# Kernel tuning notes

Measured on AMD Instinct MI355X. Metric: run time of the kernel, lower is better.

Reference implementation:

```python
import jax, jax.numpy as jnp
import numpy as np

LOC = 200 * 200 + 1   # location vocab
E = 100               # loc_emb_size
H = 100               # hidden_neurons (== input size of STLSTM)
D = 12                # temporal/spatial slot embedding dim
NSLOT = 92


def setup_inputs() -> dict:
    key = jax.random.key(0)
    ks = jax.random.split(key, 24)
    B, T = 1024, 256
    inp = {}
    inp["traj"] = jax.random.randint(ks[0], (B, T), 0, LOC)
    inp["lennew"] = jax.random.randint(ks[1], (B, T), 0, T)
    inp["traj_len"] = 255  # static scalar (loop runs traj_len+1 steps)
    inp["tu"] = jax.random.randint(ks[2], (B, T), 0, NSLOT)
    inp["tl"] = jax.random.randint(ks[3], (B, T), 0, NSLOT)
    inp["tu_slot"] = jax.random.randint(ks[4], (B, T), 0, NSLOT)
    inp["tl_slot"] = jax.random.randint(ks[5], (B, T), 0, NSLOT)
    inp["su"] = jax.random.randint(ks[6], (B, T), 0, NSLOT)
    inp["sl"] = jax.random.randint(ks[7], (B, T), 0, NSLOT)
    inp["su_slot"] = jax.random.randint(ks[8], (B, T), 0, NSLOT)
    inp["sl_slot"] = jax.random.randint(ks[9], (B, T), 0, NSLOT)
    # learned parameters
    inp["emb_loc"] = jax.random.normal(ks[10], (LOC, E), jnp.float32) * 0.02
    inp["emb_t"] = jax.random.normal(ks[11], (NSLOT, D), jnp.float32) * 0.02
    inp["emb_s"] = jax.random.normal(ks[12], (NSLOT, D), jnp.float32) * 0.02
    inp["W_ih"] = jax.random.normal(ks[13], (E, 4 * H), jnp.float32) * 0.05
    inp["W_hh"] = jax.random.normal(ks[14], (H, 4 * H), jnp.float32) * 0.05
    inp["b"] = jnp.zeros((4 * H,), jnp.float32)
    inp["W_xt"] = jax.random.normal(ks[15], (E, H), jnp.float32) * 0.05
    inp["W_tt"] = jax.random.normal(ks[16], (D, H), jnp.float32) * 0.05
    inp["b_t"] = jnp.zeros((H,), jnp.float32)
    inp["W_xs"] = jax.random.normal(ks[17], (E, H), jnp.float32) * 0.05
    inp["W_ss"] = jax.random.normal(ks[18], (D, H), jnp.float32) * 0.05
    inp["b_s"] = jnp.zeros((H,), jnp.float32)
    return inp


def reference(traj, lennew, traj_len, tu, tl, tu_slot, tl_slot, su, sl,
              su_slot, sl_slot, emb_loc, emb_t, emb_s, W_ih, W_hh, b,
              W_xt, W_tt, b_t, W_xs, W_ss, b_s):
    steps = int(traj_len) + 1  # static python int -> static slice
    x = emb_loc[traj[:, :steps]]            # [B, S, E] (dropout is identity in eval)
    dtype = x.dtype

    def interp(up_e, low_e, up_d, low_d):
        # linear interpolation between upper/lower slot embeddings
        up = up_d[:, :steps].astype(dtype)[..., None]
        low = low_d[:, :steps].astype(dtype)[..., None]
        return (up * low_e + low * up_e) / jnp.maximum(up + low, 1.0)

    Tq = interp(emb_t[tu[:, :steps]], emb_t[tl[:, :steps]], tu_slot, tl_slot)  # [B,S,D]
    Sq = interp(emb_s[su[:, :steps]], emb_s[sl[:, :steps]], su_slot, sl_slot)  # [B,S,D]

    B = traj.shape[0]
    h0 = jnp.zeros((B, H), dtype)
    c0 = jnp.zeros((B, H), dtype)
    xs = (x.swapaxes(0, 1), Tq.swapaxes(0, 1), Sq.swapaxes(0, 1))  # time-major

    def step(carry, inp):
        h, c = carry
        xt, tg, sg = inp
        gates = xt @ W_ih + h @ W_hh + b           # [B, 4H]
        i, f, g, o = jnp.split(gates, 4, axis=-1)
        i = jax.nn.sigmoid(i)
        f = jax.nn.sigmoid(f)
        g = jnp.tanh(g)
        o = jax.nn.sigmoid(o)
        tgate = jax.nn.sigmoid(xt @ W_xt + tg @ W_tt + b_t)  # temporal gate
        sgate = jax.nn.sigmoid(xt @ W_xs + sg @ W_ss + b_s)  # spatial gate
        c = f * c + i * tgate * sgate * g
        h = o * jnp.tanh(c)
        return (h, c), None

    (h, c), _ = jax.lax.scan(step, (h0, c0), xs)
    # model returns h at index traj_len, which is the final hidden state
    return h
```

## Files before the change

kernel.cpp:

```cpp
#include <hip/hip_runtime.h>

#define B_    1024
#define T_    256
#define LOCN  40001
#define E_    100
#define H_    100
#define NC    600

constexpr int PROWS = 16;
constexpr int PPAD  = 20;

__global__ __launch_bounds__(320) void proj_loc_kernel(
    const float* __restrict__ emb_loc,
    const float* __restrict__ W_ih,
    const float* __restrict__ W_xt,
    const float* __restrict__ W_xs,
    const float* __restrict__ b,
    const float* __restrict__ b_t,
    const float* __restrict__ b_s,
    float* __restrict__ P)
{
    __shared__ __attribute__((aligned(16))) float aT[E_][PPAD];
    const int tid  = threadIdx.x;
    const int row0 = blockIdx.x * PROWS;

    for (int i = tid; i < PROWS * E_; i += 320) {
        int r = i / E_, k = i - r * E_;
        int rr = row0 + r;
        float v = 0.f;
        if (rr < LOCN) v = emb_loc[rr * E_ + k];
        aT[k][r] = v;
    }
    __syncthreads();
    if (tid >= 300) return;

    for (int cc = 0; cc < 2; ++cc) {
        const int c = tid + cc * 300;
        const float* wp; int stride; float bias;
        if (c < 400)      { wp = W_ih + c;         stride = 400; bias = b[c]; }
        else if (c < 500) { wp = W_xt + (c - 400); stride = 100; bias = b_t[c - 400]; }
        else              { wp = W_xs + (c - 500); stride = 100; bias = b_s[c - 500]; }

        float acc[PROWS];
        #pragma unroll
        for (int r = 0; r < PROWS; ++r) acc[r] = bias;

        for (int k = 0; k < E_; ++k) {
            float w = wp[(size_t)k * stride];
            #pragma unroll
            for (int r = 0; r < PROWS; ++r) acc[r] += aT[k][r] * w;
        }
        #pragma unroll
        for (int r = 0; r < PROWS; ++r) {
            int rr = row0 + r;
            if (rr < LOCN) P[(size_t)rr * NC + c] = acc[r];
        }
    }
}

__global__ void proj_ts_kernel(
    const float* __restrict__ emb_t, const float* __restrict__ emb_s,
    const float* __restrict__ W_tt,  const float* __restrict__ W_ss,
    float* __restrict__ P_t, float* __restrict__ P_s)
{
    int idx = blockIdx.x * 256 + threadIdx.x;
    if (idx >= 2 * 92 * H_) return;
    int which = idx / (92 * H_);
    int rem   = idx - which * (92 * H_);
    int r = rem / H_, c = rem - r * H_;
    const float* e = which ? emb_s : emb_t;
    const float* W = which ? W_ss : W_tt;
    float acc = 0.f;
    #pragma unroll
    for (int k = 0; k < 12; ++k) acc += e[r * 12 + k] * W[k * H_ + c];
    (which ? P_s : P_t)[rem] = acc;
}

constexpr int RB = 4;
constexpr int NT = 704;

__global__ __launch_bounds__(NT, 3) void lstm_rec_kernel(
    const int* __restrict__ traj,
    const int* __restrict__ traj_len_p,
    const int* __restrict__ tu,      const int* __restrict__ tl,
    const int* __restrict__ tu_slot, const int* __restrict__ tl_slot,
    const int* __restrict__ su,      const int* __restrict__ sl,
    const int* __restrict__ su_slot, const int* __restrict__ sl_slot,
    const float* __restrict__ P,
    const float* __restrict__ P_t,
    const float* __restrict__ P_s,
    const float* __restrict__ W_hh,
    float* __restrict__ out)
{
    __shared__ __attribute__((aligned(16))) float h_lds[RB][H_];
    __shared__ float gates_lds[RB][400];
    __shared__ float tg_lds[RB][H_];
    __shared__ float sg_lds[RB][H_];
    __shared__ int   loc_lds[2][RB];

    const int tid = threadIdx.x;
    const int b0  = blockIdx.x * RB;
    int steps = traj_len_p[0] + 1;
    if (steps > T_) steps = T_;

    float w[H_];
    if (tid < 400) {
        #pragma unroll
        for (int k = 0; k < H_; ++k) w[k] = W_hh[k * 400 + tid];
        ((float*)h_lds)[tid] = 0.f;
    }
    if (tid < RB) loc_lds[0][tid] = traj[(b0 + tid) * T_];

    const int er = tid / 100;
    const int eh = tid - er * 100;
    float c_reg = 0.f, hval = 0.f;
    __syncthreads();

    for (int t = 0; t < steps; ++t) {
        const int buf = t & 1;

        if (tid >= 700) {
            int r = tid - 700;
            if (t + 1 < steps) loc_lds[buf ^ 1][r] = traj[(b0 + r) * T_ + t + 1];
        }

        if (tid < 400) {
            const int n = tid;
            float gacc[RB];
            #pragma unroll
            for (int r = 0; r < RB; ++r)
                gacc[r] = P[(size_t)loc_lds[buf][r] * NC + n];

            float acc[RB] = {0.f, 0.f, 0.f, 0.f};
            #pragma unroll
            for (int k4 = 0; k4 < H_ / 4; ++k4) {
                #pragma unroll
                for (int r = 0; r < RB; ++r) {
                    float4 hv = *(const float4*)(&h_lds[r][k4 * 4]);
                    acc[r] += hv.x * w[k4 * 4 + 0];
                    acc[r] += hv.y * w[k4 * 4 + 1];
                    acc[r] += hv.z * w[k4 * 4 + 2];
                    acc[r] += hv.w * w[k4 * 4 + 3];
                }
            }
            const bool isg = (n >= 200 && n < 300);
            #pragma unroll
            for (int r = 0; r < RB; ++r) {
                float v  = acc[r] + gacc[r];
                float xx = isg ? 2.f * v : v;
                float s  = 1.f / (1.f + expf(-xx));
                gates_lds[r][n] = isg ? (2.f * s - 1.f) : s;
            }
        }

        if (tid >= 448 && tid < 648) {
            const int  ch   = tid - 448;
            const bool is_t = ch < 100;
            const int  hx   = is_t ? ch : ch - 100;
            const int* up_a = is_t ? tu_slot : su_slot;
            const int* lo_a = is_t ? tl_slot : sl_slot;
            const int* ui_a = is_t ? tu : su;
            const int* li_a = is_t ? tl : sl;
            const float* Pq = is_t ? P_t : P_s;
            float* dst      = is_t ? &tg_lds[0][0] : &sg_lds[0][0];
            #pragma unroll
            for (int r = 0; r < RB; ++r) {
                const int off = (b0 + r) * T_ + t;
                float gp  = P[(size_t)loc_lds[buf][r] * NC + 400 + ch];
                float up  = (float)up_a[off];
                float low = (float)lo_a[off];
                int   ui  = ui_a[off], li = li_a[off];
                float iv  = (up * Pq[li * H_ + hx] + low * Pq[ui * H_ + hx])
                            / fmaxf(up + low, 1.f);
                float pre = gp + iv;
                dst[r * H_ + hx] = 1.f / (1.f + expf(-pre));
            }
        }
        __syncthreads();

        if (tid < 400) {
            float i_g = gates_lds[er][eh];
            float f_g = gates_lds[er][100 + eh];
            float g_g = gates_lds[er][200 + eh];
            float o_g = gates_lds[er][300 + eh];
            float tsg = tg_lds[er][eh] * sg_lds[er][eh];
            c_reg = f_g * c_reg + i_g * tsg * g_g;
            hval  = o_g * tanhf(c_reg);
            h_lds[er][eh] = hval;
        }
        __syncthreads();
    }

    if (tid < 400) out[b0 * H_ + tid] = hval;
}

extern "C" void kernel_launch(void* const* d_in, const int* in_sizes, int n_in,
                              void* d_out, int out_size, void* d_ws, size_t ws_size,
                              hipStream_t stream) {
    const int*   traj     = (const int*)  d_in[0];
    const int*   traj_len = (const int*)  d_in[2];
    const int*   tu       = (const int*)  d_in[3];
    const int*   tl       = (const int*)  d_in[4];
    const int*   tu_slot  = (const int*)  d_in[5];
    const int*   tl_slot  = (const int*)  d_in[6];
    const int*   su       = (const int*)  d_in[7];
    const int*   sl       = (const int*)  d_in[8];
    const int*   su_slot  = (const int*)  d_in[9];
    const int*   sl_slot  = (const int*)  d_in[10];
    const float* emb_loc  = (const float*)d_in[11];
    const float* emb_t    = (const float*)d_in[12];
    const float* emb_s    = (const float*)d_in[13];
    const float* W_ih     = (const float*)d_in[14];
    const float* W_hh     = (const float*)d_in[15];
    const float* b        = (const float*)d_in[16];
    const float* W_xt     = (const float*)d_in[17];
    const float* W_tt     = (const float*)d_in[18];
    const float* b_t      = (const float*)d_in[19];
    const float* W_xs     = (const float*)d_in[20];
    const float* W_ss     = (const float*)d_in[21];
    const float* b_s      = (const float*)d_in[22];

    float* P   = (float*)d_ws;
    float* P_t = P + (size_t)LOCN * NC;
    float* P_s = P_t + 92 * H_;

    proj_loc_kernel<<<(LOCN + PROWS - 1) / PROWS, 320, 0, stream>>>(
        emb_loc, W_ih, W_xt, W_xs, b, b_t, b_s, P);
    proj_ts_kernel<<<(2 * 92 * H_ + 255) / 256, 256, 0, stream>>>(
        emb_t, emb_s, W_tt, W_ss, P_t, P_s);
    lstm_rec_kernel<<<B_ / RB, NT, 0, stream>>>(
        traj, traj_len, tu, tl, tu_slot, tl_slot, su, sl, su_slot, sl_slot,
        P, P_t, P_s, W_hh, (float*)d_out);
}
```

Before: 830.2 us.

## Compute recurrent W_hh matvec with split-bf16 MFMA and interleave gate columns

```diff
diff --git a/kernel.cpp b/kernel.cpp
--- a/kernel.cpp
+++ b/kernel.cpp
@@ -7,16 +7,29 @@
 #define H_    100
 #define NC    600
 
+typedef __attribute__((ext_vector_type(8))) short short8;
+typedef __attribute__((ext_vector_type(4))) float f32x4;
+
+__device__ __forceinline__ float fsig(float x)  { return 1.f / (1.f + __expf(-x)); }
+__device__ __forceinline__ float ftanh(float x) { return 2.f / (1.f + __expf(-2.f * x)) - 1.f; }
+
+__device__ __forceinline__ unsigned short bf16_rne(float f) {
+    unsigned int u = __float_as_uint(f);
+    unsigned int r = u + 0x7fffu + ((u >> 16) & 1u);
+    return (unsigned short)(r >> 16);
+}
+__device__ __forceinline__ float bf16_to_f(unsigned short h) {
+    return __uint_as_float(((unsigned int)h) << 16);
+}
+
 constexpr int PROWS = 16;
 constexpr int PPAD  = 20;
 
 __global__ __launch_bounds__(320) void proj_loc_kernel(
     const float* __restrict__ emb_loc,
-    const float* __restrict__ W_ih,
-    const float* __restrict__ W_xt,
+    const float* __restrict__ W_ih, const float* __restrict__ W_xt,
     const float* __restrict__ W_xs,
-    const float* __restrict__ b,
-    const float* __restrict__ b_t,
+    const float* __restrict__ b, const float* __restrict__ b_t,
     const float* __restrict__ b_s,
     float* __restrict__ P)
 {
@@ -50,10 +63,11 @@
             #pragma unroll
             for (int r = 0; r < PROWS; ++r) acc[r] += aT[k][r] * w;
         }
+        const int cs = (c < 400) ? ((c % 100) * 4 + c / 100) : c;
         #pragma unroll
         for (int r = 0; r < PROWS; ++r) {
             int rr = row0 + r;
-            if (rr < LOCN) P[(size_t)rr * NC + c] = acc[r];
+            if (rr < LOCN) P[(size_t)rr * NC + cs] = acc[r];
         }
     }
 }
@@ -77,9 +91,10 @@
 }
 
 constexpr int RB = 4;
-constexpr int NT = 704;
-
-__global__ __launch_bounds__(NT, 3) void lstm_rec_kernel(
+constexpr int NT = 1024;
+
+__global__ __launch_bounds__(NT, 4)
+void lstm_rec_kernel(
     const int* __restrict__ traj,
     const int* __restrict__ traj_len_p,
     const int* __restrict__ tu,      const int* __restrict__ tl,
@@ -92,23 +107,44 @@
     const float* __restrict__ W_hh,
     float* __restrict__ out)
 {
-    __shared__ __attribute__((aligned(16))) float h_lds[RB][H_];
+    __shared__ __attribute__((aligned(16))) unsigned int afH32[4 * 64 * 4];
+    __shared__ __attribute__((aligned(16))) unsigned int afL32[4 * 64 * 4];
     __shared__ float gates_lds[RB][400];
     __shared__ float tg_lds[RB][H_];
     __shared__ float sg_lds[RB][H_];
     __shared__ int   loc_lds[2][RB];
 
-    const int tid = threadIdx.x;
-    const int b0  = blockIdx.x * RB;
+    const int tid  = threadIdx.x;
+    const int lane = tid & 63;
+    const int wv   = tid >> 6;
+    const int b0   = blockIdx.x * RB;
     int steps = traj_len_p[0] + 1;
     if (steps > T_) steps = T_;
 
-    float w[H_];
-    if (tid < 400) {
+    short8 bh[2][4], bl[2][4];
+    if (wv < 13) {
         #pragma unroll
-        for (int k = 0; k < H_; ++k) w[k] = W_hh[k * 400 + tid];
-        ((float*)h_lds)[tid] = 0.f;
-    }
+        for (int tt = 0; tt < 2; ++tt) {
+            const int nt = wv * 2 + tt;
+            const bool tv = (nt < 25);
+            const int n = (tv ? nt : 0) * 16 + (lane & 15);
+            #pragma unroll
+            for (int kt = 0; kt < 4; ++kt) {
+                short8 h8, l8;
+                #pragma unroll
+                for (int j = 0; j < 8; ++j) {
+                    const int k = kt * 32 + (lane >> 4) * 8 + j;
+                    const float wval = (tv && k < H_) ? W_hh[k * 400 + n] : 0.f;
+                    const unsigned short hi = bf16_rne(wval);
+                    const unsigned short lo = bf16_rne(wval - bf16_to_f(hi));
+                    h8[j] = (short)hi; l8[j] = (short)lo;
+                }
+                bh[tt][kt] = h8; bl[tt][kt] = l8;
+            }
+        }
+    }
+
+    afH32[tid] = 0u; afL32[tid] = 0u;
     if (tid < RB) loc_lds[0][tid] = traj[(b0 + tid) * T_];
 
     const int er = tid / 100;
@@ -119,74 +155,89 @@
     for (int t = 0; t < steps; ++t) {
         const int buf = t & 1;
 
-        if (tid >= 700) {
-            int r = tid - 700;
+        if (tid >= 1020) {
+            int r = tid - 1020;
             if (t + 1 < steps) loc_lds[buf ^ 1][r] = traj[(b0 + r) * T_ + t + 1];
         }
 
+        float4 pg = {0.f, 0.f, 0.f, 0.f};
         if (tid < 400) {
-            const int n = tid;
-            float gacc[RB];
+            const float4* prow = (const float4*)(P + (size_t)loc_lds[buf][er] * NC);
+            pg = prow[eh];
+        }
+
+        if (wv < 13) {
+            f32x4 acc0 = {0.f, 0.f, 0.f, 0.f};
+            f32x4 acc1 = {0.f, 0.f, 0.f, 0.f};
             #pragma unroll
-            for (int r = 0; r < RB; ++r)
-                gacc[r] = P[(size_t)loc_lds[buf][r] * NC + n];
-
-            float acc[RB] = {0.f, 0.f, 0.f, 0.f};
-            #pragma unroll
-            for (int k4 = 0; k4 < H_ / 4; ++k4) {
+            for (int kt = 0; kt < 4; ++kt) {
+                const int slot = kt * 64 + lane;
+                short8 ah = *(const short8*)&afH32[slot * 4];
+                short8 al = *(const short8*)&afL32[slot * 4];
+                acc0 = __builtin_amdgcn_mfma_f32_16x16x32_bf16(ah, bh[0][kt], acc0, 0, 0, 0);
+                acc0 = __builtin_amdgcn_mfma_f32_16x16x32_bf16(al, bh[0][kt], acc0, 0, 0, 0);
+                acc0 = __builtin_amdgcn_mfma_f32_16x16x32_bf16(ah, bl[0][kt], acc0, 0, 0, 0);
+                acc1 = __builtin_amdgcn_mfma_f32_16x16x32_bf16(ah, bh[1][kt], acc1, 0, 0, 0);
+                acc1 = __builtin_amdgcn_mfma_f32_16x16x32_bf16(al, bh[1][kt], acc1, 0, 0, 0);
+                acc1 = __builtin_amdgcn_mfma_f32_16x16x32_bf16(ah, bl[1][kt], acc1, 0, 0, 0);
+            }
+            if (lane < 16) {
+                const int col0 = (wv * 2) * 16 + lane;
+                #pragma unroll
+                for (int r = 0; r < RB; ++r) gates_lds[r][col0] = acc0[r];
+                if (wv * 2 + 1 < 25) {
+                    const int col1 = col0 + 16;
+                    #pragma unroll
+                    for (int r = 0; r < RB; ++r) gates_lds[r][col1] = acc1[r];
+                }
+            }
+        }
+
+        if (tid >= 832 && tid < 1020) {
+            for (int ch = tid - 832; ch < 200; ch += 188) {
+                const bool is_t = ch < 100;
+                const int  hx   = is_t ? ch : ch - 100;
+                const int* up_a = is_t ? tu_slot : su_slot;
+                const int* lo_a = is_t ? tl_slot : sl_slot;
+                const int* ui_a = is_t ? tu : su;
+                const int* li_a = is_t ? tl : sl;
+                const float* Pq = is_t ? P_t : P_s;
+                float* dst      = is_t ? &tg_lds[0][0] : &sg_lds[0][0];
                 #pragma unroll
                 for (int r = 0; r < RB; ++r) {
-                    float4 hv = *(const float4*)(&h_lds[r][k4 * 4]);
-                    acc[r] += hv.x * w[k4 * 4 + 0];
-                    acc[r] += hv.y * w[k4 * 4 + 1];
-                    acc[r] += hv.z * w[k4 * 4 + 2];
-                    acc[r] += hv.w * w[k4 * 4 + 3];
+                    const int off = (b0 + r) * T_ + t;
+                    float gp  = P[(size_t)loc_lds[buf][r] * NC + 400 + ch];
+                    float up  = (float)up_a[off];
+                    float low = (float)lo_a[off];
+                    int   ui  = ui_a[off], li = li_a[off];
+                    float iv  = (up * Pq[li * H_ + hx] + low * Pq[ui * H_ + hx])
+                                / fmaxf(up + low, 1.f);
+                    dst[r * H_ + hx] = fsig(gp + iv);
                 }
             }
-            const bool isg = (n >= 200 && n < 300);
-            #pragma unroll
-            for (int r = 0; r < RB; ++r) {
-                float v  = acc[r] + gacc[r];
-                float xx = isg ? 2.f * v : v;
-                float s  = 1.f / (1.f + expf(-xx));
-                gates_lds[r][n] = isg ? (2.f * s - 1.f) : s;
-            }
-        }
-
-        if (tid >= 448 && tid < 648) {
-            const int  ch   = tid - 448;
-            const bool is_t = ch < 100;
-            const int  hx   = is_t ? ch : ch - 100;
-            const int* up_a = is_t ? tu_slot : su_slot;
-            const int* lo_a = is_t ? tl_slot : sl_slot;
-            const int* ui_a = is_t ? tu : su;
-            const int* li_a = is_t ? tl : sl;
-            const float* Pq = is_t ? P_t : P_s;
-            float* dst      = is_t ? &tg_lds[0][0] : &sg_lds[0][0];
-            #pragma unroll
-            for (int r = 0; r < RB; ++r) {
-                const int off = (b0 + r) * T_ + t;
-                float gp  = P[(size_t)loc_lds[buf][r] * NC + 400 + ch];
-                float up  = (float)up_a[off];
-                float low = (float)lo_a[off];
-                int   ui  = ui_a[off], li = li_a[off];
-                float iv  = (up * Pq[li * H_ + hx] + low * Pq[ui * H_ + hx])
-                            / fmaxf(up + low, 1.f);
-                float pre = gp + iv;
-                dst[r * H_ + hx] = 1.f / (1.f + expf(-pre));
-            }
         }
         __syncthreads();
 
         if (tid < 400) {
-            float i_g = gates_lds[er][eh];
-            float f_g = gates_lds[er][100 + eh];
-            float g_g = gates_lds[er][200 + eh];
-            float o_g = gates_lds[er][300 + eh];
+            float vi = gates_lds[er][eh]       + pg.x;
+            float vf = gates_lds[er][eh + 100] + pg.y;
+            float vg = gates_lds[er][eh + 200] + pg.z;
+            float vo = gates_lds[er][eh + 300] + pg.w;
+            float ig = fsig(vi), fg = fsig(vf), gg = ftanh(vg), og = fsig(vo);
             float tsg = tg_lds[er][eh] * sg_lds[er][eh];
-            c_reg = f_g * c_reg + i_g * tsg * g_g;
-            hval  = o_g * tanhf(c_reg);
-            h_lds[er][eh] = hval;
+            c_reg = fg * c_reg + ig * tsg * gg;
+            hval  = og * ftanh(c_reg);
+
+            unsigned hb = bf16_rne(hval);
+            unsigned lb = bf16_rne(hval - bf16_to_f((unsigned short)hb));
+            unsigned hbn = (unsigned)__shfl_down((int)hb, 1);
+            unsigned lbn = (unsigned)__shfl_down((int)lb, 1);
+            if ((eh & 1) == 0) {
+                const int slot = (eh >> 5) * 64 + er + (((eh >> 3) & 3) << 4);
+                const int didx = slot * 4 + ((eh & 7) >> 1);
+                afH32[didx] = hb | (hbn << 16);
+                afL32[didx] = lb | (lbn << 16);
+            }
         }
         __syncthreads();
     }
```

Result: slower. 1.325 ms (+59.6%).
